# Kernel tuning notes

Hardware: AMD Instinct MI355X
Metric: run time of the kernel (lower is better)

Reference implementation:

```python
import jax, jax.numpy as jnp
import numpy as np

LN_EPS = 1e-5

def _layernorm(x, g, b):
    mu = jnp.mean(x, axis=-1, keepdims=True)
    var = jnp.var(x, axis=-1, keepdims=True)
    return (x - mu) / jnp.sqrt(var + LN_EPS) * g + b

def setup_inputs() -> dict:
    key = jax.random.key(0)
    ks = jax.random.split(key, 12)
    N, D_WSI, D_OMIC, D, DH = 50000, 1024, 1577, 256, 128
    def rn(k, shape, s=0.02):
        return jax.random.normal(k, shape, jnp.float32) * s
    return {
        'wsi': jax.random.normal(ks[0], (N, D_WSI), jnp.float32),
        'x_omic': jax.random.normal(ks[1], (D_OMIC,), jnp.float32),
        # SNNOmics: Linear(1577,256)+ELU, Linear(256,256)+ELU (AlphaDropout=eval identity)
        'W1': rn(ks[2], (D_OMIC, 256)), 'b1': jnp.zeros((256,), jnp.float32),
        'W2': rn(ks[3], (256, 256)), 'b2': jnp.zeros((256,), jnp.float32),
        # wsi projection Linear(1024,256)
        'Wp': rn(ks[4], (D_WSI, D)), 'bp': jnp.zeros((D,), jnp.float32),
        # MMAttentionLayer pre-norm (dim=256)
        'ln1_g': jnp.ones((D,), jnp.float32), 'ln1_b': jnp.zeros((D,), jnp.float32),
        # to_qkv: Linear(256, 3*heads*dim_head) = Linear(256, 384), no bias (heads=1, dim_head=128)
        'Wqkv': rn(ks[5], (D, 3 * DH)),
        # FeedForward(dim=128, mult=1): LN + Linear(128,128)+GELU+Linear(128,128) (no residual)
        'ln2_g': jnp.ones((DH,), jnp.float32), 'ln2_b': jnp.zeros((DH,), jnp.float32),
        'Wf1': rn(ks[6], (DH, DH)), 'bf1': jnp.zeros((DH,), jnp.float32),
        'Wf2': rn(ks[7], (DH, DH)), 'bf2': jnp.zeros((DH,), jnp.float32),
        # final LayerNorm(128)
        'ln3_g': jnp.ones((DH,), jnp.float32), 'ln3_b': jnp.zeros((DH,), jnp.float32),
        # to_logits: Linear(256,64)+ReLU+Linear(64,4)
        'Wl1': rn(ks[8], (2 * DH, 64)), 'bl1': jnp.zeros((64,), jnp.float32),
        'Wl2': rn(ks[9], (64, 4)), 'bl2': jnp.zeros((4,), jnp.float32),
    }

def reference(wsi, x_omic, W1, b1, W2, b2, Wp, bp, ln1_g, ln1_b, Wqkv,
              ln2_g, ln2_b, Wf1, bf1, Wf2, bf2, ln3_g, ln3_b, Wl1, bl1, Wl2, bl2):
    M = 1            # num_pathways
    DH = 128         # dim_head (heads=1)
    scale = DH ** -0.5
    # SNN omics encoder -> one pathway token [1, 256]
    h = jax.nn.elu(x_omic @ W1 + b1)
    h = jax.nn.elu(h @ W2 + b2)
    h_omic = h[None, :]                              # [1, 256]
    # WSI projection -> histology tokens [N, 256]
    wsi_embed = wsi @ Wp + bp                        # [N, 256]
    tokens = jnp.concatenate([h_omic, wsi_embed], axis=0)   # [1+N, 256]
    # MMAttentionLayer: pre-norm then asymmetric pathway/histology attention
    xn = _layernorm(tokens, ln1_g, ln1_b)
    qkv = xn @ Wqkv                                  # [1+N, 384]
    q, k, v = jnp.split(qkv, 3, axis=-1)             # each [1+N, 128]
    q = q * scale
    q_p, q_h = q[:M], q[M:]                          # [1,128], [N,128]
    k_p, k_h = k[:M], k[M:]
    # cross attention: histology -> pathways (rows of length M=1)
    cross_attn_hist = q_h @ k_p.T                    # [N, 1]
    cross_attn_hist = jax.nn.softmax(cross_attn_hist, axis=-1)
    # pathway row attends to [pathways | histology]
    attn_p = q_p @ k_p.T                             # [1, 1]
    cross_attn_p = q_p @ k_h.T                       # [1, N]
    attn_ph = jax.nn.softmax(jnp.concatenate([attn_p, cross_attn_p], axis=-1), axis=-1)  # [1, 1+N]
    out_p = attn_ph @ v                              # [1, 128]
    out_h = cross_attn_hist @ v[:M]                  # [N, 128]
    out = jnp.concatenate([out_p, out_h], axis=0)    # [1+N, 128] (residual=False: no conv)
    # FeedForward (no residual add in original) + LayerNorm
    mm = _layernorm(out, ln2_g, ln2_b)
    mm = jax.nn.gelu(mm @ Wf1 + bf1, approximate=False) @ Wf2 + bf2
    mm = _layernorm(mm, ln3_g, ln3_b)                # [1+N, 128]
    paths_embed = jnp.mean(mm[:M], axis=0)           # [128]
    wsi_embed_post = jnp.mean(mm[M:], axis=0)        # [128]
    embedding = jnp.concatenate([paths_embed, wsi_embed_post])[None, :]  # [1, 256]
    logits = jax.nn.relu(embedding @ Wl1 + bl1) @ Wl2 + bl2              # [1, 4]
    prob = jax.nn.softmax(logits, axis=-1)
    return logits, prob
```

## Files before the change

### kernel.cpp

```cpp
#include <hip/hip_runtime.h>
#include <hip/hip_bf16.h>
#include <math.h>

#define LN_EPS 1e-5f

typedef unsigned short ushortT;
typedef short bf16x8 __attribute__((ext_vector_type(8)));
typedef float f32x4 __attribute__((ext_vector_type(4)));

#define WS_QP   0
#define WS_V0   128
#define WS_S0   256
#define WS_LL   258
#define WS_E0   259
#define WS_H1P  512
#define WS_PART 4608
#define PART_STRIDE 132
#define PART_M 128
#define PART_L 129
#define WS_WTS  108000
#define WS_GP   109000
#define NCOMB   32
#define WS_WPT  131072
#define WS_WKVT 262144

__device__ __forceinline__ float elu1(float x){ return x > 0.f ? x : expm1f(x); }
__device__ __forceinline__ unsigned short f2bf(float x){
  unsigned u = __float_as_uint(x);
  return (unsigned short)((u + 0x7fffu + ((u >> 16) & 1u)) >> 16);
}
__device__ __forceinline__ unsigned pk2(float lo, float hi){
  union { __hip_bfloat162 h; unsigned u; } cv;
  cv.h = __float22bfloat162_rn(make_float2(lo, hi));
  return cv.u;
}
__device__ __forceinline__ void dma16(const void* g, void* l) {
  __builtin_amdgcn_global_load_lds(
      (const __attribute__((address_space(1))) unsigned int*)g,
      (__attribute__((address_space(3))) unsigned int*)l, 16, 0, 0);
}
template<int N> __device__ __forceinline__ void vwait() {
  asm volatile("s_waitcnt vmcnt(%0)" :: "i"(N) : "memory");
}
__device__ __forceinline__ void lwait0() {
  asm volatile("s_waitcnt lgkmcnt(0)" ::: "memory");
}
__device__ __forceinline__ void sbar()   { __builtin_amdgcn_s_barrier(); }
__device__ __forceinline__ void schedb() { __builtin_amdgcn_sched_barrier(0); }

__global__ __launch_bounds__(256) void k_prep(const float* __restrict__ Wp,
    const float* __restrict__ Wqkv, ushortT* __restrict__ wpt, ushortT* __restrict__ wkvt)
{
  int bb = blockIdx.x, t = threadIdx.x;
  if (bb < 256) {
    int k0 = bb * 4;
    unsigned lo, hi;
    lo = (unsigned)f2bf(Wp[(size_t)(k0 + 0) * 256 + t]) |
         ((unsigned)f2bf(Wp[(size_t)(k0 + 1) * 256 + t]) << 16);
    hi = (unsigned)f2bf(Wp[(size_t)(k0 + 2) * 256 + t]) |
         ((unsigned)f2bf(Wp[(size_t)(k0 + 3) * 256 + t]) << 16);
    *(uint2*)&wpt[t * 1024 + k0] = make_uint2(lo, hi);
  } else {
    int k0 = (bb - 256) * 4;
    unsigned lo, hi;
    lo = (unsigned)f2bf(Wqkv[(size_t)(k0 + 0) * 384 + 128 + t]) |
         ((unsigned)f2bf(Wqkv[(size_t)(k0 + 1) * 384 + 128 + t]) << 16);
    hi = (unsigned)f2bf(Wqkv[(size_t)(k0 + 2) * 384 + 128 + t]) |
         ((unsigned)f2bf(Wqkv[(size_t)(k0 + 3) * 384 + 128 + t]) << 16);
    *(uint2*)&wkvt[t * 256 + k0] = make_uint2(lo, hi);
  }
}

__global__ __launch_bounds__(256) void k_h1(const float* __restrict__ x,
    const float* __restrict__ W1, int d_omic, float* __restrict__ ws)
{
  int g = blockIdx.x, tid = threadIdx.x;
  int i0 = g * 99, i1 = min(i0 + 99, d_omic);
  __shared__ float xs[112];
  for (int i = i0 + tid; i < i1; i += 256) xs[i - i0] = x[i];
  __syncthreads();
  float s = 0.f;
  for (int i = i0; i < i1; i++) s = fmaf(xs[i - i0], W1[(size_t)i * 256 + tid], s);
  ws[WS_H1P + g * 256 + tid] = s;
}

__global__ __launch_bounds__(256) void k_omic(
    const float* __restrict__ b1,
    const float* __restrict__ W2, const float* __restrict__ b2,
    const float* __restrict__ Wqkv,
    const float* __restrict__ ln1_g, const float* __restrict__ ln1_b,
    float* __restrict__ ws)
{
  __shared__ float h1[256];
  __shared__ float xn0[256];
  __shared__ float qs[128], ks[128];
  __shared__ float red[8];
  int tid = threadIdx.x, lane = tid & 63, wave = tid >> 6;

  float s = b1[tid];
  for (int g = 0; g < 16; g++) s += ws[WS_H1P + g * 256 + tid];
  h1[tid] = elu1(s);
  __syncthreads();

  s = b2[tid];
  for (int i = 0; i < 256; i++) s = fmaf(h1[i], W2[i * 256 + tid], s);
  float t0 = elu1(s);

  float ps = t0, pq = t0 * t0;
  for (int m = 1; m < 64; m <<= 1) { ps += __shfl_xor(ps, m); pq += __shfl_xor(pq, m); }
  if (lane == 0) { red[wave] = ps; red[4 + wave] = pq; }
  __syncthreads();
  float mu = (red[0] + red[1] + red[2] + red[3]) * (1.f / 256.f);
  float var = (red[4] + red[5] + red[6] + red[7]) * (1.f / 256.f) - mu * mu;
  float xn = (t0 - mu) * rsqrtf(var + LN_EPS) * ln1_g[tid] + ln1_b[tid];
  xn0[tid] = xn;
  __syncthreads();

  float a = 0.f;
  for (int j = 0; j < 256; j++) a = fmaf(xn0[j], Wqkv[j * 384 + tid], a);
  if (tid < 128) { float q = a * 0.088388347648318447f; qs[tid] = q; ws[WS_QP + tid] = q; }
  else           { ks[tid - 128] = a; }
  if (tid < 128) {
    float av = 0.f;
    for (int j = 0; j < 256; j++) av = fmaf(xn0[j], Wqkv[j * 384 + 256 + tid], av);
    ws[WS_V0 + tid] = av;
  }
  __syncthreads();
  float p = (tid < 128) ? qs[tid] * ks[tid] : 0.f;
  for (int m = 1; m < 64; m <<= 1) p += __shfl_xor(p, m);
  if (lane == 0) red[wave] = p;
  __syncthreads();
  if (tid == 0) ws[WS_S0] = red[0] + red[1] + red[2] + red[3];
}

__global__ __launch_bounds__(256, 2) void k_main(
    const float* __restrict__ wsi, int N,
    const ushortT* __restrict__ wpt, const ushortT* __restrict__ wkvt,
    const float* __restrict__ bp,
    const float* __restrict__ ln1_g, const float* __restrict__ ln1_b,
    float* __restrict__ ws)
{
  __shared__ __align__(16) char SW[3 * 16384];
  __shared__ __align__(16) char SS[3 * 8192];
  __shared__ float wtsL[64];

  const int tid = threadIdx.x;
  const int lane = tid & 63, wv = tid >> 6;
  const int l15 = lane & 15, lh = lane >> 4;
  const int b = blockIdx.x, r0 = b * 64;

  int wsrc[2];
  #pragma unroll
  for (int i = 0; i < 2; ++i) {
    int row = 16 * wv + 8 * i + (lane >> 3);
    int c   = lane & 7;
    int gr  = r0 + row; gr = (gr < N) ? gr : (N - 1);
    wsrc[i] = gr * 1024 + ((c ^ (row & 7)) << 2);
  }
  int psrc[4], kvsrc[4];
  #pragma unroll
  for (int j = 0; j < 4; ++j) {
    int p  = lane >> 3;
    int cc = (lane & 7) ^ (p & 7);
    int mj = 16 * j + 2 * p + (cc >> 2);
    int m  = 64 * wv + mj;
    int c  = cc & 3;
    psrc[j]  = m * 1024 + c * 8;
    kvsrc[j] = m * 256  + c * 8;
  }
  const unsigned afc = (unsigned)(((4 * (l15 & 1) + lh) ^ (l15 >> 1)) << 4);
  const unsigned bc0 = (unsigned)(((2 * lh)     ^ (l15 & 7)) << 4);
  const unsigned bc1 = (unsigned)(((2 * lh + 1) ^ (l15 & 7)) << 4);

  const f32x4 z4 = {0.f, 0.f, 0.f, 0.f};
  f32x4 acc[4][4];
  #pragma unroll
  for (int mt = 0; mt < 4; ++mt)
    #pragma unroll
    for (int nt = 0; nt < 4; ++nt) acc[mt][nt] = z4;

  auto stageP1 = [&](int kc, int slot) {
    char* ds = SS + slot * 8192 + wv * 2048;
    #pragma unroll
    for (int i = 0; i < 2; ++i) dma16(wsi + wsrc[i] + kc * 32, ds + i * 1024);
    char* dw = SW + slot * 16384 + wv * 4096;
    #pragma unroll
    for (int j = 0; j < 4; ++j) dma16(wpt + psrc[j] + kc * 32, dw + j * 1024);
  };
  auto computeP1 = [&](int slot) {
    const char* Wb = SW + slot * 16384 + wv * 4096;
    const char* Sb = SS + slot * 8192;
    bf16x8 af[4], bfr[4];
    #pragma unroll
    for (int mt = 0; mt < 4; ++mt)
      af[mt] = *(const bf16x8*)(Wb + (8 * mt + (l15 >> 1)) * 128 + afc);
    #pragma unroll
    for (int nt = 0; nt < 4; ++nt) {
      const char* p = Sb + (l15 + 16 * nt) * 128;
      uint4 ua = *(const uint4*)(p + bc0);
      uint4 ub = *(const uint4*)(p + bc1);
      union { unsigned u[4]; bf16x8 v; } cv;
      cv.u[0] = pk2(__uint_as_float(ua.x), __uint_as_float(ua.y));
      cv.u[1] = pk2(__uint_as_float(ua.z), __uint_as_float(ua.w));
      cv.u[2] = pk2(__uint_as_float(ub.x), __uint_as_float(ub.y));
      cv.u[3] = pk2(__uint_as_float(ub.z), __uint_as_float(ub.w));
      bfr[nt] = cv.v;
    }
    #pragma unroll
    for (int mt = 0; mt < 4; ++mt)
      #pragma unroll
      for (int nt = 0; nt < 4; ++nt)
        acc[mt][nt] = __builtin_amdgcn_mfma_f32_16x16x32_bf16(af[mt], bfr[nt], acc[mt][nt], 0, 0, 0);
  };

  stageP1(0, 0); stageP1(1, 1); stageP1(2, 2);
  int slot = 0;
  for (int kc = 0; kc < 32; ++kc) {
    if (kc < 30) vwait<12>(); else if (kc == 30) vwait<6>(); else vwait<0>();
    sbar(); schedb();
    computeP1(slot);
    sbar(); schedb();
    if (kc < 29) stageP1(kc + 3, slot);
    slot = (slot == 2) ? 0 : slot + 1;
  }

  auto stageKV = [&](int t) {
    char* dst = ((t & 1) ? SS : SW + 32768) + wv * 4096;
    #pragma unroll
    for (int j = 0; j < 4; ++j) dma16(wkvt + kvsrc[j] + t * 32, dst + j * 1024);
  };
  stageKV(0); stageKV(1);

  float* red = (float*)(SS + 16384);
  float4 bp4[4], g4[4], b4[4];
  #pragma unroll
  for (int mt = 0; mt < 4; ++mt) {
    int m0 = 64 * wv + 16 * mt + 4 * lh;
    bp4[mt] = *(const float4*)&bp[m0];
    g4[mt]  = *(const float4*)&ln1_g[m0];
    b4[mt]  = *(const float4*)&ln1_b[m0];
  }
  float ps[4], pq[4];
  #pragma unroll
  for (int nt = 0; nt < 4; ++nt) { ps[nt] = 0.f; pq[nt] = 0.f; }
  #pragma unroll
  for (int mt = 0; mt < 4; ++mt) {
    const float bb4[4] = {bp4[mt].x, bp4[mt].y, bp4[mt].z, bp4[mt].w};
    #pragma unroll
    for (int nt = 0; nt < 4; ++nt)
      #pragma unroll
      for (int r = 0; r < 4; ++r) {
        float v = acc[mt][nt][r] + bb4[r];
        acc[mt][nt][r] = v;
        ps[nt] += v; pq[nt] += v * v;
      }
  }
  #pragma unroll
  for (int nt = 0; nt < 4; ++nt) {
    ps[nt] += __shfl_xor(ps[nt], 16); pq[nt] += __shfl_xor(pq[nt], 16);
    ps[nt] += __shfl_xor(ps[nt], 32); pq[nt] += __shfl_xor(pq[nt], 32);
  }
  if (lh == 0) {
    #pragma unroll
    for (int nt = 0; nt < 4; ++nt) {
      int row = l15 + 16 * nt;
      red[(wv * 64 + row) * 2]     = ps[nt];
      red[(wv * 64 + row) * 2 + 1] = pq[nt];
    }
  }
  lwait0(); sbar(); schedb();
  float mu[4], rstd[4];
  #pragma unroll
  for (int nt = 0; nt < 4; ++nt) {
    int row = l15 + 16 * nt;
    float s_ = 0.f, q_ = 0.f;
    #pragma unroll
    for (int w2 = 0; w2 < 4; ++w2) { s_ += red[(w2 * 64 + row) * 2]; q_ += red[(w2 * 64 + row) * 2 + 1]; }
    float m_ = s_ * (1.f / 256.f);
    float v_ = q_ * (1.f / 256.f) - m_ * m_;
    mu[nt] = m_; rstd[nt] = rsqrtf(v_ + LN_EPS);
  }
  #pragma unroll
  for (int nt = 0; nt < 4; ++nt) {
    int row = l15 + 16 * nt;
    unsigned rswz = (unsigned)((row & 7) << 4);
    #pragma unroll
    for (int mt = 0; mt < 4; ++mt) {
      float x0 = (acc[mt][nt][0] - mu[nt]) * rstd[nt] * g4[mt].x + b4[mt].x;
      float x1 = (acc[mt][nt][1] - mu[nt]) * rstd[nt] * g4[mt].y + b4[mt].y;
      float x2 = (acc[mt][nt][2] - mu[nt]) * rstd[nt] * g4[mt].z + b4[mt].z;
      float x3 = (acc[mt][nt][3] - mu[nt]) * rstd[nt] * g4[mt].w + b4[mt].w;
      unsigned p0 = pk2(x0, x1);
      unsigned p1 = pk2(x2, x3);
      int m0 = 64 * wv + 16 * mt + 4 * lh;
      unsigned off = (unsigned)(row * 512 + m0 * 2) ^ rswz;
      *(uint2*)(SW + off) = make_uint2(p0, p1);
    }
  }
  lwait0(); sbar(); schedb();

  f32x4 acc2[4][4];
  #pragma unroll
  for (int mt = 0; mt < 4; ++mt)
    #pragma unroll
    for (int nt = 0; nt < 4; ++nt) acc2[mt][nt] = z4;

  for (int kk = 0; kk < 8; ++kk) {
    if (kk < 7) vwait<4>(); else vwait<0>();
    sbar(); schedb();
    {
      const char* Pb = ((kk & 1) ? SS : SW + 32768) + wv * 4096;
      bf16x8 af[4], bfr[4];
      #pragma unroll
      for (int mt = 0; mt < 4; ++mt)
        af[mt] = *(const bf16x8*)(Pb + (8 * mt + (l15 >> 1)) * 128 + afc);
      #pragma unroll
      for (int nt = 0; nt < 4; ++nt) {
        int row = l15 + 16 * nt;
        unsigned off = (unsigned)(row * 512 + lh * 16 + kk * 64) ^ (unsigned)((row & 7) << 4);
        bfr[nt] = *(const bf16x8*)(SW + off);
      }
      #pragma unroll
      for (int mt = 0; mt < 4; ++mt)
        #pragma unroll
        for (int nt = 0; nt < 4; ++nt)
          acc2[mt][nt] = __builtin_amdgcn_mfma_f32_16x16x32_bf16(af[mt], bfr[nt], acc2[mt][nt], 0, 0, 0);
    }
    sbar(); schedb();
    if (kk < 6) stageKV(kk + 2);
  }

  float* part = ws + WS_PART + (size_t)b * PART_STRIDE;

  if (wv < 2) {
    float4 qp4[4];
    #pragma unroll
    for (int mt = 0; mt < 4; ++mt)
      qp4[mt] = *(const float4*)&ws[WS_QP + 64 * wv + 16 * mt + 4 * lh];
    float sp[4];
    #pragma unroll
    for (int nt = 0; nt < 4; ++nt) {
      float s_ = 0.f;
      #pragma unroll
      for (int mt = 0; mt < 4; ++mt) {
        s_ = fmaf(qp4[mt].x, acc2[mt][nt][0], s_);
        s_ = fmaf(qp4[mt].y, acc2[mt][nt][1], s_);
        s_ = fmaf(qp4[mt].z, acc2[mt][nt][2], s_);
        s_ = fmaf(qp4[mt].w, acc2[mt][nt][3], s_);
      }
      sp[nt] = s_;
    }
    #pragma unroll
    for (int nt = 0; nt < 4; ++nt) {
      sp[nt] += __shfl_xor(sp[nt], 16);
      sp[nt] += __shfl_xor(sp[nt], 32);
    }
    if (lh == 0) {
      #pragma unroll
      for (int nt = 0; nt < 4; ++nt) red[wv * 64 + 16 * nt + l15] = sp[nt];
    }
  }
  __syncthreads();
  if (tid < 64) {
    int gr = r0 + tid;
    float s_ = red[tid] + red[64 + tid];
    if (gr >= N) s_ = -INFINITY;
    float mb = s_;
    #pragma unroll
    for (int m = 1; m < 64; m <<= 1) mb = fmaxf(mb, __shfl_xor(mb, m));
    float e = (gr < N) ? expf(s_ - mb) : 0.f;
    float l_ = e;
    #pragma unroll
    for (int m = 1; m < 64; m <<= 1) l_ += __shfl_xor(l_, m);
    wtsL[tid] = e;
    if (tid == 0) { part[PART_M] = mb; part[PART_L] = l_; }
  }
  __syncthreads();
  if (wv >= 2) {
    int wv2 = wv - 2;
    float wr[4];
    #pragma unroll
    for (int nt = 0; nt < 4; ++nt) wr[nt] = wtsL[16 * nt + l15];
    #pragma unroll
    for (int mt = 0; mt < 4; ++mt) {
      float vs0 = 0.f, vs1 = 0.f, vs2 = 0.f, vs3 = 0.f;
      #pragma unroll
      for (int nt = 0; nt < 4; ++nt) {
        vs0 = fmaf(wr[nt], acc2[mt][nt][0], vs0);
        vs1 = fmaf(wr[nt], acc2[mt][nt][1], vs1);
        vs2 = fmaf(wr[nt], acc2[mt][nt][2], vs2);
        vs3 = fmaf(wr[nt], acc2[mt][nt][3], vs3);
      }
      #pragma unroll
      for (int m = 1; m < 16; m <<= 1) {
        vs0 += __shfl_xor(vs0, m); vs1 += __shfl_xor(vs1, m);
        vs2 += __shfl_xor(vs2, m); vs3 += __shfl_xor(vs3, m);
      }
      if (l15 == 0)
        *(float4*)&part[64 * wv2 + 16 * mt + 4 * lh] = make_float4(vs0, vs1, vs2, vs3);
    }
  }
}

__global__ __launch_bounds__(256) void k_fin0(float* __restrict__ ws, int NB)
{
  __shared__ float red[8];
  int tid = threadIdx.x, lane = tid & 63, wave = tid >> 6;
  const float* part = ws + WS_PART;
  float s0 = ws[WS_S0];

  float mloc = s0;
  for (int bb = tid; bb < NB; bb += 256) mloc = fmaxf(mloc, part[(size_t)bb * PART_STRIDE + PART_M]);
  for (int m = 1; m < 64; m <<= 1) mloc = fmaxf(mloc, __shfl_xor(mloc, m));
  if (lane == 0) red[wave] = mloc;
  __syncthreads();
  float M = fmaxf(fmaxf(red[0], red[1]), fmaxf(red[2], red[3]));

  float lp = 0.f;
  for (int bb = tid; bb < NB; bb += 256) {
    float w = expf(part[(size_t)bb * PART_STRIDE + PART_M] - M);
    ws[WS_WTS + bb] = w;
    lp = fmaf(part[(size_t)bb * PART_STRIDE + PART_L], w, lp);
  }
  for (int m = 1; m < 64; m <<= 1) lp += __shfl_xor(lp, m);
  __syncthreads();
  if (lane == 0) red[wave] = lp;
  __syncthreads();
  if (tid == 0) {
    float e0 = expf(s0 - M);
    ws[WS_LL] = red[0] + red[1] + red[2] + red[3] + e0;
    ws[WS_E0] = e0;
  }
}

__global__ __launch_bounds__(128) void k_fin1(float* __restrict__ ws, int NB, int chunk)
{
  int g = blockIdx.x, col = threadIdx.x;
  int c0 = g * chunk, c1 = min(c0 + chunk, NB);
  const float* part = ws + WS_PART;
  const float* wts = ws + WS_WTS;
  float a = 0.f;
  #pragma unroll 4
  for (int bb = c0; bb < c1; ++bb)
    a = fmaf(part[(size_t)bb * PART_STRIDE + col], wts[bb], a);
  ws[WS_GP + g * 128 + col] = a;
}

__global__ __launch_bounds__(256) void k_final(
    const float* __restrict__ ws,
    const float* __restrict__ Wf1, const float* __restrict__ bf1,
    const float* __restrict__ Wf2, const float* __restrict__ bf2,
    const float* __restrict__ ln2_g, const float* __restrict__ ln2_b,
    const float* __restrict__ ln3_g, const float* __restrict__ ln3_b,
    const float* __restrict__ Wl1, const float* __restrict__ bl1,
    const float* __restrict__ Wl2, const float* __restrict__ bl2,
    float* __restrict__ out)
{
  __shared__ float rowb[2][128];
  __shared__ float mmb[2][128];
  __shared__ float red[8];
  __shared__ float emb[256];
  __shared__ float abuf[64];
  __shared__ float lbuf[4];
  int tid = threadIdx.x, lane = tid & 63, wave = tid >> 6;

  if (tid < 128) {
    float v0 = ws[WS_V0 + tid];
    float a = v0 * ws[WS_E0];
    #pragma unroll
    for (int g = 0; g < NCOMB; ++g) a += ws[WS_GP + g * 128 + tid];
    rowb[0][tid] = a / ws[WS_LL];
    rowb[1][tid] = v0;
  }
  __syncthreads();

  int row = tid >> 7, k = tid & 127;
  float x = rowb[row][k];
  float ps = x, pq = x * x;
  for (int m = 1; m < 64; m <<= 1) { ps += __shfl_xor(ps, m); pq += __shfl_xor(pq, m); }
  __syncthreads();
  if (lane == 0) { red[wave] = ps; red[4 + wave] = pq; }
  __syncthreads();
  {
    float sum = red[row * 2] + red[row * 2 + 1];
    float sq  = red[4 + row * 2] + red[4 + row * 2 + 1];
    float mu = sum * (1.f / 128.f);
    float var = sq * (1.f / 128.f) - mu * mu;
    x = (x - mu) * rsqrtf(var + LN_EPS) * ln2_g[k] + ln2_b[k];
  }
  mmb[row][k] = x;
  __syncthreads();
  float t1 = bf1[k];
  for (int j = 0; j < 128; j++) t1 = fmaf(mmb[row][j], Wf1[j * 128 + k], t1);
  float gg = t1 * 0.5f * (1.f + erff(t1 * 0.70710678118654752f));
  __syncthreads();
  rowb[row][k] = gg;
  __syncthreads();
  float t2 = bf2[k];
  for (int j = 0; j < 128; j++) t2 = fmaf(rowb[row][j], Wf2[j * 128 + k], t2);
  ps = t2; pq = t2 * t2;
  for (int m = 1; m < 64; m <<= 1) { ps += __shfl_xor(ps, m); pq += __shfl_xor(pq, m); }
  __syncthreads();
  if (lane == 0) { red[wave] = ps; red[4 + wave] = pq; }
  __syncthreads();
  {
    float sum = red[row * 2] + red[row * 2 + 1];
    float sq  = red[4 + row * 2] + red[4 + row * 2 + 1];
    float mu = sum * (1.f / 128.f);
    float var = sq * (1.f / 128.f) - mu * mu;
    t2 = (t2 - mu) * rsqrtf(var + LN_EPS) * ln3_g[k] + ln3_b[k];
  }
  emb[row * 128 + k] = t2;
  __syncthreads();
  if (tid < 64) {
    float a = bl1[tid];
    for (int j = 0; j < 256; j++) a = fmaf(emb[j], Wl1[j * 64 + tid], a);
    abuf[tid] = fmaxf(a, 0.f);
  }
  __syncthreads();
  if (tid < 4) {
    float lg = bl2[tid];
    for (int j = 0; j < 64; j++) lg = fmaf(abuf[j], Wl2[j * 4 + tid], lg);
    lbuf[tid] = lg;
  }
  __syncthreads();
  if (tid < 4) {
    float m4 = fmaxf(fmaxf(lbuf[0], lbuf[1]), fmaxf(lbuf[2], lbuf[3]));
    float e0 = expf(lbuf[0] - m4), e1 = expf(lbuf[1] - m4);
    float e2 = expf(lbuf[2] - m4), e3 = expf(lbuf[3] - m4);
    float ssum = e0 + e1 + e2 + e3;
    out[tid] = lbuf[tid];
    out[4 + tid] = expf(lbuf[tid] - m4) / ssum;
  }
}

extern "C" void kernel_launch(void* const* d_in, const int* in_sizes, int n_in,
                              void* d_out, int out_size, void* d_ws, size_t ws_size,
                              hipStream_t stream) {
  const float* wsi    = (const float*)d_in[0];
  const float* x_omic = (const float*)d_in[1];
  const float* W1     = (const float*)d_in[2];
  const float* b1     = (const float*)d_in[3];
  const float* W2     = (const float*)d_in[4];
  const float* b2     = (const float*)d_in[5];
  const float* Wp     = (const float*)d_in[6];
  const float* bp     = (const float*)d_in[7];
  const float* ln1_g  = (const float*)d_in[8];
  const float* ln1_b  = (const float*)d_in[9];
  const float* Wqkv   = (const float*)d_in[10];
  const float* ln2_g  = (const float*)d_in[11];
  const float* ln2_b  = (const float*)d_in[12];
  const float* Wf1    = (const float*)d_in[13];
  const float* bf1    = (const float*)d_in[14];
  const float* Wf2    = (const float*)d_in[15];
  const float* bf2    = (const float*)d_in[16];
  const float* ln3_g  = (const float*)d_in[17];
  const float* ln3_b  = (const float*)d_in[18];
  const float* Wl1    = (const float*)d_in[19];
  const float* bl1    = (const float*)d_in[20];
  const float* Wl2    = (const float*)d_in[21];
  const float* bl2    = (const float*)d_in[22];
  float* ws   = (float*)d_ws;
  float* outp = (float*)d_out;
  ushortT* wpt  = (ushortT*)(ws + WS_WPT);
  ushortT* wkvt = (ushortT*)(ws + WS_WKVT);

  int N = in_sizes[0] / 1024;
  int d_omic = in_sizes[1];
  int NB = (N + 63) / 64;
  int chunk = (NB + NCOMB - 1) / NCOMB;

  k_prep<<<320, 256, 0, stream>>>(Wp, Wqkv, wpt, wkvt);
  k_h1<<<16, 256, 0, stream>>>(x_omic, W1, d_omic, ws);
  k_omic<<<1, 256, 0, stream>>>(b1, W2, b2, Wqkv, ln1_g, ln1_b, ws);
  k_main<<<NB, 256, 0, stream>>>(wsi, N, wpt, wkvt, bp, ln1_g, ln1_b, ws);
  k_fin0<<<1, 256, 0, stream>>>(ws, NB);
  k_fin1<<<NCOMB, 128, 0, stream>>>(ws, NB, chunk);
  k_final<<<1, 256, 0, stream>>>(ws, Wf1, bf1, Wf2, bf2, ln2_g, ln2_b,
                                 ln3_g, ln3_b, Wl1, bl1, Wl2, bl2, outp);
}
```

Baseline: 162.3 us.

## Double wsi tile to 128 rows with 8-wave blocks and pre-swizzled bf16 weights

The main kernel now processes 128 wsi rows per block using 512 threads (2 row groups by 4 column groups). This halves the number of times the projection weights are streamed per row. Weights are pre-packed into a k-sliced, swizzled bf16 layout so each slice loads with contiguous DMA. The pipeline changes from triple to double buffering, and the KV GEMM now reads its A operand straight from global/L2 instead of staging it in LDS. The prep and omic-h1 kernels are merged into one launch, and the softmax and V reductions gain cross-row-group LDS reductions and extra barriers.

```diff
diff --git a/kernel.cpp b/kernel.cpp
--- a/kernel.cpp
+++ b/kernel.cpp
@@ -25,10 +25,6 @@
 #define WS_WKVT 262144
 
 __device__ __forceinline__ float elu1(float x){ return x > 0.f ? x : expm1f(x); }
-__device__ __forceinline__ unsigned short f2bf(float x){
-  unsigned u = __float_as_uint(x);
-  return (unsigned short)((u + 0x7fffu + ((u >> 16) & 1u)) >> 16);
-}
 __device__ __forceinline__ unsigned pk2(float lo, float hi){
   union { __hip_bfloat162 h; unsigned u; } cv;
   cv.h = __float22bfloat162_rn(make_float2(lo, hi));
@@ -48,40 +44,42 @@
 __device__ __forceinline__ void sbar()   { __builtin_amdgcn_s_barrier(); }
 __device__ __forceinline__ void schedb() { __builtin_amdgcn_sched_barrier(0); }
 
-__global__ __launch_bounds__(256) void k_prep(const float* __restrict__ Wp,
-    const float* __restrict__ Wqkv, ushortT* __restrict__ wpt, ushortT* __restrict__ wkvt)
+__global__ __launch_bounds__(256) void k_setup(
+    const float* __restrict__ Wp, const float* __restrict__ Wqkv,
+    const float* __restrict__ x, const float* __restrict__ W1, int d_omic,
+    ushortT* __restrict__ wpt, ushortT* __restrict__ wkvt, float* __restrict__ ws)
 {
   int bb = blockIdx.x, t = threadIdx.x;
-  if (bb < 256) {
-    int k0 = bb * 4;
-    unsigned lo, hi;
-    lo = (unsigned)f2bf(Wp[(size_t)(k0 + 0) * 256 + t]) |
-         ((unsigned)f2bf(Wp[(size_t)(k0 + 1) * 256 + t]) << 16);
-    hi = (unsigned)f2bf(Wp[(size_t)(k0 + 2) * 256 + t]) |
-         ((unsigned)f2bf(Wp[(size_t)(k0 + 3) * 256 + t]) << 16);
-    *(uint2*)&wpt[t * 1024 + k0] = make_uint2(lo, hi);
+  if (bb < 32) {
+    int kc = bb, m = t, sw = (m >> 1) & 3;
+    #pragma unroll
+    for (int c = 0; c < 4; ++c) {
+      float v[8];
+      #pragma unroll
+      for (int e = 0; e < 8; ++e) v[e] = Wp[(size_t)(kc * 32 + c * 8 + e) * 256 + m];
+      uint4 w = make_uint4(pk2(v[0], v[1]), pk2(v[2], v[3]), pk2(v[4], v[5]), pk2(v[6], v[7]));
+      *(uint4*)&wpt[kc * 8192 + m * 32 + ((c ^ sw) * 8)] = w;
+    }
+  } else if (bb < 40) {
+    int kk = bb - 32, m = t, sw = (m >> 1) & 3;
+    #pragma unroll
+    for (int c = 0; c < 4; ++c) {
+      float v[8];
+      #pragma unroll
+      for (int e = 0; e < 8; ++e) v[e] = Wqkv[(size_t)(kk * 32 + c * 8 + e) * 384 + 128 + m];
+      uint4 w = make_uint4(pk2(v[0], v[1]), pk2(v[2], v[3]), pk2(v[4], v[5]), pk2(v[6], v[7]));
+      *(uint4*)&wkvt[kk * 8192 + m * 32 + ((c ^ sw) * 8)] = w;
+    }
   } else {
-    int k0 = (bb - 256) * 4;
-    unsigned lo, hi;
-    lo = (unsigned)f2bf(Wqkv[(size_t)(k0 + 0) * 384 + 128 + t]) |
-         ((unsigned)f2bf(Wqkv[(size_t)(k0 + 1) * 384 + 128 + t]) << 16);
-    hi = (unsigned)f2bf(Wqkv[(size_t)(k0 + 2) * 384 + 128 + t]) |
-         ((unsigned)f2bf(Wqkv[(size_t)(k0 + 3) * 384 + 128 + t]) << 16);
-    *(uint2*)&wkvt[t * 256 + k0] = make_uint2(lo, hi);
-  }
-}
-
-__global__ __launch_bounds__(256) void k_h1(const float* __restrict__ x,
-    const float* __restrict__ W1, int d_omic, float* __restrict__ ws)
-{
-  int g = blockIdx.x, tid = threadIdx.x;
-  int i0 = g * 99, i1 = min(i0 + 99, d_omic);
-  __shared__ float xs[112];
-  for (int i = i0 + tid; i < i1; i += 256) xs[i - i0] = x[i];
-  __syncthreads();
-  float s = 0.f;
-  for (int i = i0; i < i1; i++) s = fmaf(xs[i - i0], W1[(size_t)i * 256 + tid], s);
-  ws[WS_H1P + g * 256 + tid] = s;
+    int g = bb - 40;
+    int i0 = g * 99, i1 = min(i0 + 99, d_omic);
+    __shared__ float xs[112];
+    for (int i = i0 + t; i < i1; i += 256) xs[i - i0] = x[i];
+    __syncthreads();
+    float s = 0.f;
+    for (int i = i0; i < i1; i++) s = fmaf(xs[i - i0], W1[(size_t)i * 256 + t], s);
+    ws[WS_H1P + g * 256 + t] = s;
+  }
 }
 
 __global__ __launch_bounds__(256) void k_omic(
@@ -133,44 +131,36 @@
   if (tid == 0) ws[WS_S0] = red[0] + red[1] + red[2] + red[3];
 }
 
-__global__ __launch_bounds__(256, 2) void k_main(
+__global__ __launch_bounds__(512, 4) void k_main(
     const float* __restrict__ wsi, int N,
     const ushortT* __restrict__ wpt, const ushortT* __restrict__ wkvt,
     const float* __restrict__ bp,
     const float* __restrict__ ln1_g, const float* __restrict__ ln1_b,
     float* __restrict__ ws)
 {
-  __shared__ __align__(16) char SW[3 * 16384];
-  __shared__ __align__(16) char SS[3 * 8192];
-  __shared__ float wtsL[64];
+  __shared__ __align__(16) char U[65536];
+  char* Uw = U + 32768;
 
   const int tid = threadIdx.x;
   const int lane = tid & 63, wv = tid >> 6;
   const int l15 = lane & 15, lh = lane >> 4;
-  const int b = blockIdx.x, r0 = b * 64;
-
-  int wsrc[2];
+  const int cg = wv & 3, rg = wv >> 2;
+  const int b = blockIdx.x, r0 = b * 128;
+
+  int wsiSrc[2];
   #pragma unroll
   for (int i = 0; i < 2; ++i) {
-    int row = 16 * wv + 8 * i + (lane >> 3);
-    int c   = lane & 7;
-    int gr  = r0 + row; gr = (gr < N) ? gr : (N - 1);
-    wsrc[i] = gr * 1024 + ((c ^ (row & 7)) << 2);
-  }
-  int psrc[4], kvsrc[4];
-  #pragma unroll
-  for (int j = 0; j < 4; ++j) {
-    int p  = lane >> 3;
-    int cc = (lane & 7) ^ (p & 7);
-    int mj = 16 * j + 2 * p + (cc >> 2);
-    int m  = 64 * wv + mj;
-    int c  = cc & 3;
-    psrc[j]  = m * 1024 + c * 8;
-    kvsrc[j] = m * 256  + c * 8;
-  }
-  const unsigned afc = (unsigned)(((4 * (l15 & 1) + lh) ^ (l15 >> 1)) << 4);
-  const unsigned bc0 = (unsigned)(((2 * lh)     ^ (l15 & 7)) << 4);
-  const unsigned bc1 = (unsigned)(((2 * lh + 1) ^ (l15 & 7)) << 4);
+    int rowL = 16 * wv + 8 * i + (lane >> 3);
+    int gr = r0 + rowL; gr = (gr < N) ? gr : (N - 1);
+    wsiSrc[i] = gr * 1024 + (((lane & 7) ^ (lane >> 3)) << 2);
+  }
+  int wptSrc[2];
+  #pragma unroll
+  for (int j = 0; j < 2; ++j) wptSrc[j] = (32 * wv + 16 * j) * 32 + lane * 8;
+
+  const unsigned afslot = (unsigned)((lh ^ ((l15 >> 1) & 3)) << 4);
+  const unsigned bs0 = (unsigned)(((2 * lh)     ^ (l15 & 7)) << 4);
+  const unsigned bs1 = (unsigned)(((2 * lh + 1) ^ (l15 & 7)) << 4);
 
   const f32x4 z4 = {0.f, 0.f, 0.f, 0.f};
   f32x4 acc[4][4];
@@ -179,63 +169,53 @@
     #pragma unroll
     for (int nt = 0; nt < 4; ++nt) acc[mt][nt] = z4;
 
-  auto stageP1 = [&](int kc, int slot) {
-    char* ds = SS + slot * 8192 + wv * 2048;
-    #pragma unroll
-    for (int i = 0; i < 2; ++i) dma16(wsi + wsrc[i] + kc * 32, ds + i * 1024);
-    char* dw = SW + slot * 16384 + wv * 4096;
-    #pragma unroll
-    for (int j = 0; j < 4; ++j) dma16(wpt + psrc[j] + kc * 32, dw + j * 1024);
+  auto dmaSlice = [&](int kc, int k) {
+    char* ds = U + k * 16384 + wv * 2048;
+    #pragma unroll
+    for (int i = 0; i < 2; ++i) dma16(wsi + wsiSrc[i] + kc * 32, ds + i * 1024);
+    char* dw = Uw + k * 16384 + wv * 2048;
+    #pragma unroll
+    for (int j = 0; j < 2; ++j) dma16(wpt + wptSrc[j] + kc * 8192, dw + j * 1024);
   };
-  auto computeP1 = [&](int slot) {
-    const char* Wb = SW + slot * 16384 + wv * 4096;
-    const char* Sb = SS + slot * 8192;
-    bf16x8 af[4], bfr[4];
-    #pragma unroll
-    for (int mt = 0; mt < 4; ++mt)
-      af[mt] = *(const bf16x8*)(Wb + (8 * mt + (l15 >> 1)) * 128 + afc);
-    #pragma unroll
-    for (int nt = 0; nt < 4; ++nt) {
-      const char* p = Sb + (l15 + 16 * nt) * 128;
-      uint4 ua = *(const uint4*)(p + bc0);
-      uint4 ub = *(const uint4*)(p + bc1);
-      union { unsigned u[4]; bf16x8 v; } cv;
-      cv.u[0] = pk2(__uint_as_float(ua.x), __uint_as_float(ua.y));
-      cv.u[1] = pk2(__uint_as_float(ua.z), __uint_as_float(ua.w));
-      cv.u[2] = pk2(__uint_as_float(ub.x), __uint_as_float(ub.y));
-      cv.u[3] = pk2(__uint_as_float(ub.z), __uint_as_float(ub.w));
-      bfr[nt] = cv.v;
-    }
-    #pragma unroll
-    for (int mt = 0; mt < 4; ++mt)
-      #pragma unroll
-      for (int nt = 0; nt < 4; ++nt)
-        acc[mt][nt] = __builtin_amdgcn_mfma_f32_16x16x32_bf16(af[mt], bfr[nt], acc[mt][nt], 0, 0, 0);
-  };
-
-  stageP1(0, 0); stageP1(1, 1); stageP1(2, 2);
-  int slot = 0;
-  for (int kc = 0; kc < 32; ++kc) {
-    if (kc < 30) vwait<12>(); else if (kc == 30) vwait<6>(); else vwait<0>();
+
+  dmaSlice(0, 0);
+  for (int s = 0; s < 32; ++s) {
+    if (s < 31) { dmaSlice(s + 1, (s + 1) & 1); vwait<4>(); }
+    else vwait<0>();
     sbar(); schedb();
-    computeP1(slot);
+    {
+      const char* Ws = U  + (s & 1) * 16384;
+      const char* Wf = Uw + (s & 1) * 16384;
+      bf16x8 af[4], bfr[4];
+      #pragma unroll
+      for (int mt = 0; mt < 4; ++mt)
+        af[mt] = *(const bf16x8*)(Wf + (64 * cg + 16 * mt + l15) * 64 + afslot);
+      #pragma unroll
+      for (int nt = 0; nt < 4; ++nt) {
+        const char* p = Ws + (64 * rg + 16 * nt + l15) * 128;
+        uint4 ua = *(const uint4*)(p + bs0);
+        uint4 ub = *(const uint4*)(p + bs1);
+        union { unsigned u[4]; bf16x8 v; } cv;
+        cv.u[0] = pk2(__uint_as_float(ua.x), __uint_as_float(ua.y));
+        cv.u[1] = pk2(__uint_as_float(ua.z), __uint_as_float(ua.w));
+        cv.u[2] = pk2(__uint_as_float(ub.x), __uint_as_float(ub.y));
+        cv.u[3] = pk2(__uint_as_float(ub.z), __uint_as_float(ub.w));
+        bfr[nt] = cv.v;
+      }
+      #pragma unroll
+      for (int mt = 0; mt < 4; ++mt)
+        #pragma unroll
+        for (int nt = 0; nt < 4; ++nt)
+          acc[mt][nt] = __builtin_amdgcn_mfma_f32_16x16x32_bf16(af[mt], bfr[nt], acc[mt][nt], 0, 0, 0);
+    }
     sbar(); schedb();
-    if (kc < 29) stageP1(kc + 3, slot);
-    slot = (slot == 2) ? 0 : slot + 1;
-  }
-
-  auto stageKV = [&](int t) {
-    char* dst = ((t & 1) ? SS : SW + 32768) + wv * 4096;
-    #pragma unroll
-    for (int j = 0; j < 4; ++j) dma16(wkvt + kvsrc[j] + t * 32, dst + j * 1024);
-  };
-  stageKV(0); stageKV(1);
-
-  float* red = (float*)(SS + 16384);
+  }
+
+  float* red = (float*)U;
   float4 bp4[4], g4[4], b4[4];
   #pragma unroll
   for (int mt = 0; mt < 4; ++mt) {
-    int m0 = 64 * wv + 16 * mt + 4 * lh;
+    int m0 = 64 * cg + 16 * mt + 4 * lh;
     bp4[mt] = *(const float4*)&bp[m0];
     g4[mt]  = *(const float4*)&ln1_g[m0];
     b4[mt]  = *(const float4*)&ln1_b[m0];
@@ -263,26 +243,27 @@
   if (lh == 0) {
     #pragma unroll
     for (int nt = 0; nt < 4; ++nt) {
-      int row = l15 + 16 * nt;
-      red[(wv * 64 + row) * 2]     = ps[nt];
-      red[(wv * 64 + row) * 2 + 1] = pq[nt];
+      int row = 64 * rg + 16 * nt + l15;
+      *(float2*)&red[row * 8 + cg * 2] = make_float2(ps[nt], pq[nt]);
     }
   }
   lwait0(); sbar(); schedb();
   float mu[4], rstd[4];
   #pragma unroll
   for (int nt = 0; nt < 4; ++nt) {
-    int row = l15 + 16 * nt;
+    int row = 64 * rg + 16 * nt + l15;
     float s_ = 0.f, q_ = 0.f;
     #pragma unroll
-    for (int w2 = 0; w2 < 4; ++w2) { s_ += red[(w2 * 64 + row) * 2]; q_ += red[(w2 * 64 + row) * 2 + 1]; }
+    for (int c = 0; c < 4; ++c) { s_ += red[row * 8 + c * 2]; q_ += red[row * 8 + c * 2 + 1]; }
     float m_ = s_ * (1.f / 256.f);
     float v_ = q_ * (1.f / 256.f) - m_ * m_;
     mu[nt] = m_; rstd[nt] = rsqrtf(v_ + LN_EPS);
   }
+  lwait0(); sbar(); schedb();
+
   #pragma unroll
   for (int nt = 0; nt < 4; ++nt) {
-    int row = l15 + 16 * nt;
+    int row = 64 * rg + 16 * nt + l15;
     unsigned rswz = (unsigned)((row & 7) << 4);
     #pragma unroll
     for (int mt = 0; mt < 4; ++mt) {
@@ -290,11 +271,8 @@
       float x1 = (acc[mt][nt][1] - mu[nt]) * rstd[nt] * g4[mt].y + b4[mt].y;
       float x2 = (acc[mt][nt][2] - mu[nt]) * rstd[nt] * g4[mt].z + b4[mt].z;
       float x3 = (acc[mt][nt][3] - mu[nt]) * rstd[nt] * g4[mt].w + b4[mt].w;
-      unsigned p0 = pk2(x0, x1);
-      unsigned p1 = pk2(x2, x3);
-      int m0 = 64 * wv + 16 * mt + 4 * lh;
-      unsigned off = (unsigned)(row * 512 + m0 * 2) ^ rswz;
-      *(uint2*)(SW + off) = make_uint2(p0, p1);
+      unsigned off = (unsigned)(row * 512 + (64 * cg + 16 * mt + 4 * lh) * 2) ^ rswz;
+      *(uint2*)(U + off) = make_uint2(pk2(x0, x1), pk2(x2, x3));
     }
   }
   lwait0(); sbar(); schedb();
@@ -304,39 +282,68 @@
   for (int mt = 0; mt < 4; ++mt)
     #pragma unroll
     for (int nt = 0; nt < 4; ++nt) acc2[mt][nt] = z4;
-
-  for (int kk = 0; kk < 8; ++kk) {
-    if (kk < 7) vwait<4>(); else vwait<0>();
-    sbar(); schedb();
+  int kvBase[4];
+  #pragma unroll
+  for (int mt = 0; mt < 4; ++mt) {
+    int m = 64 * cg + 16 * mt + l15;
+    kvBase[mt] = m * 32 + ((lh ^ ((m >> 1) & 3)) << 3);
+  }
+  bf16x8 gA[4], gB[4];
+  #pragma unroll
+  for (int mt = 0; mt < 4; ++mt) gA[mt] = *(const bf16x8*)(wkvt + kvBase[mt]);
+  #pragma unroll
+  for (int kp = 0; kp < 4; ++kp) {
+    const int kk0 = 2 * kp, kk1 = 2 * kp + 1;
+    #pragma unroll
+    for (int mt = 0; mt < 4; ++mt)
+      gB[mt] = *(const bf16x8*)(wkvt + kvBase[mt] + kk1 * 8192);
     {
-      const char* Pb = ((kk & 1) ? SS : SW + 32768) + wv * 4096;
-      bf16x8 af[4], bfr[4];
-      #pragma unroll
-      for (int mt = 0; mt < 4; ++mt)
-        af[mt] = *(const bf16x8*)(Pb + (8 * mt + (l15 >> 1)) * 128 + afc);
+      bf16x8 bfr[4];
       #pragma unroll
       for (int nt = 0; nt < 4; ++nt) {
-        int row = l15 + 16 * nt;
-        unsigned off = (unsigned)(row * 512 + lh * 16 + kk * 64) ^ (unsigned)((row & 7) << 4);
-        bfr[nt] = *(const bf16x8*)(SW + off);
+        int row = 64 * rg + 16 * nt + l15;
+        unsigned off = (unsigned)(row * 512 + kk0 * 64 + lh * 16) ^ (unsigned)((row & 7) << 4);
+        bfr[nt] = *(const bf16x8*)(U + off);
       }
       #pragma unroll
       for (int mt = 0; mt < 4; ++mt)
         #pragma unroll
         for (int nt = 0; nt < 4; ++nt)
-          acc2[mt][nt] = __builtin_amdgcn_mfma_f32_16x16x32_bf16(af[mt], bfr[nt], acc2[mt][nt], 0, 0, 0);
-    }
-    sbar(); schedb();
-    if (kk < 6) stageKV(kk + 2);
-  }
-
+          acc2[mt][nt] = __builtin_amdgcn_mfma_f32_16x16x32_bf16(gA[mt], bfr[nt], acc2[mt][nt], 0, 0, 0);
+    }
+    if (kp < 3) {
+      #pragma unroll
+      for (int mt = 0; mt < 4; ++mt)
+        gA[mt] = *(const bf16x8*)(wkvt + kvBase[mt] + (kk0 + 2) * 8192);
+    }
+    {
+      bf16x8 bfr[4];
+      #pragma unroll
+      for (int nt = 0; nt < 4; ++nt) {
+        int row = 64 * rg + 16 * nt + l15;
+        unsigned off = (unsigned)(row * 512 + kk1 * 64 + lh * 16) ^ (unsigned)((row & 7) << 4);
+        bfr[nt] = *(const bf16x8*)(U + off);
+      }
+      #pragma unroll
+      for (int mt = 0; mt < 4; ++mt)
+        #pragma unroll
+        for (int nt = 0; nt < 4; ++nt)
+          acc2[mt][nt] = __builtin_amdgcn_mfma_f32_16x16x32_bf16(gB[mt], bfr[nt], acc2[mt][nt], 0, 0, 0);
+    }
+  }
+  sbar(); schedb();
+
+  float* sred = (float*)U;
+  float* aux  = (float*)(U + 1024);
+  float* wts  = (float*)(U + 1056);
+  float* vred = (float*)(U + 1600);
   float* part = ws + WS_PART + (size_t)b * PART_STRIDE;
 
-  if (wv < 2) {
+  if (cg < 2) {
     float4 qp4[4];
     #pragma unroll
     for (int mt = 0; mt < 4; ++mt)
-      qp4[mt] = *(const float4*)&ws[WS_QP + 64 * wv + 16 * mt + 4 * lh];
+      qp4[mt] = *(const float4*)&ws[WS_QP + 64 * cg + 16 * mt + 4 * lh];
     float sp[4];
     #pragma unroll
     for (int nt = 0; nt < 4; ++nt) {
@@ -357,30 +364,34 @@
     }
     if (lh == 0) {
       #pragma unroll
-      for (int nt = 0; nt < 4; ++nt) red[wv * 64 + 16 * nt + l15] = sp[nt];
-    }
-  }
-  __syncthreads();
-  if (tid < 64) {
-    int gr = r0 + tid;
-    float s_ = red[tid] + red[64 + tid];
-    if (gr >= N) s_ = -INFINITY;
-    float mb = s_;
-    #pragma unroll
-    for (int m = 1; m < 64; m <<= 1) mb = fmaxf(mb, __shfl_xor(mb, m));
-    float e = (gr < N) ? expf(s_ - mb) : 0.f;
-    float l_ = e;
-    #pragma unroll
-    for (int m = 1; m < 64; m <<= 1) l_ += __shfl_xor(l_, m);
-    wtsL[tid] = e;
-    if (tid == 0) { part[PART_M] = mb; part[PART_L] = l_; }
-  }
-  __syncthreads();
-  if (wv >= 2) {
-    int wv2 = wv - 2;
+      for (int nt = 0; nt < 4; ++nt) sred[cg * 128 + 64 * rg + 16 * nt + l15] = sp[nt];
+    }
+  }
+  lwait0(); sbar(); schedb();
+
+  float sv = -INFINITY, ev = 0.f;
+  if (tid < 128) {
+    sv = sred[tid] + sred[128 + tid];
+    if (r0 + tid >= N) sv = -INFINITY;
+  }
+  float mb = sv;
+  #pragma unroll
+  for (int m = 1; m < 64; m <<= 1) mb = fmaxf(mb, __shfl_xor(mb, m));
+  if (tid < 128 && lane == 0) aux[tid >> 6] = mb;
+  lwait0(); sbar(); schedb();
+  float M2 = fmaxf(aux[0], aux[1]);
+  if (tid < 128) { ev = (r0 + tid < N) ? expf(sv - M2) : 0.f; wts[tid] = ev; }
+  float lsum = ev;
+  #pragma unroll
+  for (int m = 1; m < 64; m <<= 1) lsum += __shfl_xor(lsum, m);
+  if (tid < 128 && lane == 0) aux[2 + (tid >> 6)] = lsum;
+  lwait0(); sbar(); schedb();
+  if (tid == 0) { part[PART_M] = M2; part[PART_L] = aux[2] + aux[3]; }
+
+  if (cg >= 2) {
     float wr[4];
     #pragma unroll
-    for (int nt = 0; nt < 4; ++nt) wr[nt] = wtsL[16 * nt + l15];
+    for (int nt = 0; nt < 4; ++nt) wr[nt] = wts[64 * rg + 16 * nt + l15];
     #pragma unroll
     for (int mt = 0; mt < 4; ++mt) {
       float vs0 = 0.f, vs1 = 0.f, vs2 = 0.f, vs3 = 0.f;
@@ -397,9 +408,12 @@
         vs2 += __shfl_xor(vs2, m); vs3 += __shfl_xor(vs3, m);
       }
       if (l15 == 0)
-        *(float4*)&part[64 * wv2 + 16 * mt + 4 * lh] = make_float4(vs0, vs1, vs2, vs3);
-    }
-  }
+        *(float4*)&vred[128 * rg + 64 * (cg - 2) + 16 * mt + 4 * lh] =
+            make_float4(vs0, vs1, vs2, vs3);
+    }
+  }
+  lwait0(); sbar(); schedb();
+  if (tid < 128) part[tid] = vred[tid] + vred[128 + tid];
 }
 
 __global__ __launch_bounds__(256) void k_fin0(float* __restrict__ ws, int NB)
@@ -567,13 +581,12 @@
 
   int N = in_sizes[0] / 1024;
   int d_omic = in_sizes[1];
-  int NB = (N + 63) / 64;
+  int NB = (N + 127) / 128;
   int chunk = (NB + NCOMB - 1) / NCOMB;
 
-  k_prep<<<320, 256, 0, stream>>>(Wp, Wqkv, wpt, wkvt);
-  k_h1<<<16, 256, 0, stream>>>(x_omic, W1, d_omic, ws);
+  k_setup<<<56, 256, 0, stream>>>(Wp, Wqkv, x_omic, W1, d_omic, wpt, wkvt, ws);
   k_omic<<<1, 256, 0, stream>>>(b1, W2, b2, Wqkv, ln1_g, ln1_b, ws);
-  k_main<<<NB, 256, 0, stream>>>(wsi, N, wpt, wkvt, bp, ln1_g, ln1_b, ws);
+  k_main<<<NB, 512, 0, stream>>>(wsi, N, wpt, wkvt, bp, ln1_g, ln1_b, ws);
   k_fin0<<<1, 256, 0, stream>>>(ws, NB);
   k_fin1<<<NCOMB, 128, 0, stream>>>(ws, NB, chunk);
   k_final<<<1, 256, 0, stream>>>(ws, Wf1, bf1, Wf2, bf2, ln2_g, ln2_b,
```

After: 131.8 us. 18.8% less time.
